# Performance work log

Measured on AMD Instinct MI355X. Metric: run time of the kernel, lower is better.

Reference implementation:

```python
import jax, jax.numpy as jnp
import numpy as np

N_NODES = 50000
N_EDGES = 800000
D_IN, D1, D2, D_OUT = 128, 150, 100, 64


def setup_inputs() -> dict:
    key = jax.random.key(0)
    ks = jax.random.split(key, 10)
    x = jax.random.normal(ks[0], (N_NODES, D_IN), dtype=jnp.float32)
    src = jax.random.randint(ks[1], (N_EDGES,), 0, N_NODES, dtype=jnp.int32)
    dst = jax.random.randint(ks[2], (N_EDGES,), 0, N_NODES, dtype=jnp.int32)
    s1 = 1.0 / np.sqrt(D_IN)
    s2 = 1.0 / np.sqrt(D1)
    s3 = 1.0 / np.sqrt(D2)
    W1 = jax.random.uniform(ks[3], (D_IN, D1), jnp.float32, -s1, s1)
    b1 = jnp.zeros((D1,), jnp.float32)
    Wn = jax.random.uniform(ks[4], (D1, D2), jnp.float32, -s2, s2)
    Ws = jax.random.uniform(ks[5], (D1, D2), jnp.float32, -s2, s2)
    b2 = jnp.zeros((D2,), jnp.float32)
    W3 = jax.random.uniform(ks[6], (D2, D_OUT), jnp.float32, -s3, s3)
    b3 = jnp.zeros((D_OUT,), jnp.float32)
    return {"x": x, "src": src, "dst": dst, "W1": W1, "b1": b1,
            "Wn": Wn, "Ws": Ws, "b2": b2, "W3": W3, "b3": b3}


def _degrees(src, dst, n):
    ones = jnp.ones(src.shape[0], jnp.float32)
    deg_out = jax.ops.segment_sum(ones, src, num_segments=n)
    deg_in = jax.ops.segment_sum(ones, dst, num_segments=n)
    return deg_out, deg_in


def reference(x, src, dst, W1, b1, Wn, Ws, b2, W3, b3):
    n = x.shape[0]
    deg_out, deg_in = _degrees(src, dst, n)
    norm_out = jax.lax.rsqrt(jnp.maximum(deg_out, 1.0))  # [N]
    norm_in = jax.lax.rsqrt(jnp.maximum(deg_in, 1.0))    # [N]

    # --- GraphConv (norm='both'): D_in^{-1/2} A D_out^{-1/2} X W + b ---
    h = x * norm_out[:, None]                                   # [N, D_IN]
    agg = jax.ops.segment_sum(h[src], dst, num_segments=n)      # [N, D_IN]
    h = (agg * norm_in[:, None]) @ W1 + b1                      # [N, D1]
    h = jax.nn.elu(h)

    # --- SAGEConv (mean): fc_self(h) + fc_neigh(mean_neighbors(h)) + b ---
    neigh_sum = jax.ops.segment_sum(h[src], dst, num_segments=n)  # [N, D1]
    neigh = neigh_sum / jnp.maximum(deg_in, 1.0)[:, None]
    h = h @ Ws + neigh @ Wn + b2                                  # [N, D2]
    h = jax.nn.elu(h)

    # --- Dense + ELU ---
    out = jax.nn.elu(h @ W3 + b3)                                 # [N, D_OUT]
    return out
```

## Files before the change

### kernel.cpp

```cpp
#include <hip/hip_runtime.h>
#include <math.h>

#define N_NODES 50000
#define N_EDGES 800000
#define D_IN 128
#define D1 150
#define LD1 152
#define D2 100
#define LDP 128
#define D_OUT 64
#define SLOT 64
#define HBLK 64
#define HBIN 12500

#define LDS_K 40

using short8 = __attribute__((ext_vector_type(8))) short;
using f32x4  = __attribute__((ext_vector_type(4))) float;

__device__ __forceinline__ float elu(float v) { return v > 0.0f ? v : expm1f(v); }

__device__ __forceinline__ void split_bf16(float a, unsigned short& h, unsigned short& l) {
    unsigned int bits = __float_as_uint(a);
    unsigned int hb = (bits + 0x8000u) >> 16;
    h = (unsigned short)hb;
    float r = a - __uint_as_float(hb << 16);
    l = (unsigned short)((__float_as_uint(r) + 0x8000u) >> 16);
}

__device__ __forceinline__ void split_store16(unsigned short* hrow, unsigned short* lrow,
                                              const float* vv) {
    short8 h0, h1v, l0, l1v;
#pragma unroll
    for (int i = 0; i < 8; ++i) {
        unsigned short hh, ll;
        split_bf16(vv[i], hh, ll);
        h0[i] = (short)hh; l0[i] = (short)ll;
    }
#pragma unroll
    for (int i = 0; i < 8; ++i) {
        unsigned short hh, ll;
        split_bf16(vv[8 + i], hh, ll);
        h1v[i] = (short)hh; l1v[i] = (short)ll;
    }
    *(short8*)(hrow) = h0;
    *(short8*)(hrow + 8) = h1v;
    *(short8*)(lrow) = l0;
    *(short8*)(lrow + 8) = l1v;
}

__global__ __launch_bounds__(256) void hist_kernel(const int* __restrict__ src,
                                                   unsigned int* __restrict__ partial) {
    __shared__ unsigned int bins[HBIN];
    int tid = threadIdx.x, b = blockIdx.x;
    for (int i = tid; i < HBIN; i += 256) bins[i] = 0u;
    __syncthreads();
    int e0 = b * (N_EDGES / HBLK);
    int e1 = e0 + (N_EDGES / HBLK);
    for (int e = e0 + tid; e < e1; e += 256) {
        int s = src[e];
        atomicAdd(&bins[s >> 2], 1u << ((s & 3) * 8));
    }
    __syncthreads();
    unsigned int* outp = partial + (size_t)b * HBIN;
    for (int i = tid; i < HBIN; i += 256) outp[i] = bins[i];
}

__global__ __launch_bounds__(256) void norm_kernel(const unsigned int* __restrict__ partial,
                                                   float* __restrict__ norm_out) {
    int i = blockIdx.x * blockDim.x + threadIdx.x;
    if (i >= HBIN) return;
    unsigned int acc = 0;
#pragma unroll
    for (int h = 0; h < HBLK; ++h) acc += partial[(size_t)h * HBIN + i];
#pragma unroll
    for (int j = 0; j < 4; ++j) {
        unsigned int dg = (acc >> (j * 8)) & 0xFF;
        norm_out[i * 4 + j] = rsqrtf(fmaxf((float)dg, 1.0f));
    }
}

__global__ void fill_kernel(const int* __restrict__ src, const int* __restrict__ dst,
                            int* __restrict__ cursor, unsigned short* __restrict__ slots) {
    int e = blockIdx.x * blockDim.x + threadIdx.x;
    if (e < N_EDGES) {
        int d = dst[e], s = src[e];
        int pos = atomicAdd(&cursor[d], 1);
        if (pos < SLOT) slots[d * SLOT + pos] = (unsigned short)s;
    }
}

__global__ __launch_bounds__(256) void gather_x(const float* __restrict__ x,
                                                const float* __restrict__ norm_out,
                                                const int* __restrict__ deg_in,
                                                const unsigned short* __restrict__ slots,
                                                float* __restrict__ agg) {
    int wave = threadIdx.x >> 6;
    int lane = threadIdx.x & 63;
    int half = lane >> 5;
    int c = lane & 31;
    int n = blockIdx.x * 4 + wave;
    if (n >= N_NODES) return;
    int beg = n * SLOT;
    int dg = deg_in[n]; if (dg > SLOT) dg = SLOT;
    int end = beg + dg;
    float4 acc = {0.0f, 0.0f, 0.0f, 0.0f};
    int e = beg + half;
    for (; e + 2 < end; e += 4) {
        int s0 = slots[e];
        int s1 = slots[e + 2];
        float w0 = norm_out[s0], w1 = norm_out[s1];
        float4 v0 = ((const float4*)(x + (size_t)s0 * D_IN))[c];
        float4 v1 = ((const float4*)(x + (size_t)s1 * D_IN))[c];
        acc.x += v0.x * w0 + v1.x * w1;
        acc.y += v0.y * w0 + v1.y * w1;
        acc.z += v0.z * w0 + v1.z * w1;
        acc.w += v0.w * w0 + v1.w * w1;
    }
    if (e < end) {
        int s = slots[e];
        float w = norm_out[s];
        float4 v = ((const float4*)(x + (size_t)s * D_IN))[c];
        acc.x += v.x * w; acc.y += v.y * w; acc.z += v.z * w; acc.w += v.w * w;
    }
    acc.x += __shfl_xor(acc.x, 32);
    acc.y += __shfl_xor(acc.y, 32);
    acc.z += __shfl_xor(acc.z, 32);
    acc.w += __shfl_xor(acc.w, 32);
    if (half == 0) ((float4*)(agg + (size_t)n * D_IN))[c] = acc;
}

__global__ __launch_bounds__(256) void gather_p(const float* __restrict__ p,
                                                const int* __restrict__ deg_in,
                                                const unsigned short* __restrict__ slots,
                                                float* __restrict__ ns) {
    int wave = threadIdx.x >> 6;
    int lane = threadIdx.x & 63;
    int half = lane >> 5;
    int c = lane & 31;
    bool cv = c < D2 / 4;
    int n = blockIdx.x * 4 + wave;
    if (n >= N_NODES) return;
    int beg = n * SLOT;
    int dg = deg_in[n]; if (dg > SLOT) dg = SLOT;
    int end = beg + dg;
    float4 acc = {0.0f, 0.0f, 0.0f, 0.0f};
    if (cv) {
        int e = beg + half;
        for (; e + 2 < end; e += 4) {
            int s0 = slots[e];
            int s1 = slots[e + 2];
            float4 v0 = ((const float4*)(p + (size_t)s0 * LDP))[c];
            float4 v1 = ((const float4*)(p + (size_t)s1 * LDP))[c];
            acc.x += v0.x + v1.x;
            acc.y += v0.y + v1.y;
            acc.z += v0.z + v1.z;
            acc.w += v0.w + v1.w;
        }
        if (e < end) {
            int s = slots[e];
            float4 v = ((const float4*)(p + (size_t)s * LDP))[c];
            acc.x += v.x; acc.y += v.y; acc.z += v.z; acc.w += v.w;
        }
    }
    acc.x += __shfl_xor(acc.x, 32);
    acc.y += __shfl_xor(acc.y, 32);
    acc.z += __shfl_xor(acc.z, 32);
    acc.w += __shfl_xor(acc.w, 32);
    if (half == 0 && cv) ((float4*)(ns + (size_t)n * LDP))[c] = acc;
}


template <int K, int KP, int NW, int LDA, int PRE, int EPI, int LDC, int GROUP>
__global__ __launch_bounds__(256, PRE ? 2 : 3)
void gemm_mfma(const float* __restrict__ A, const float* __restrict__ W,
               const float* __restrict__ nsrc, const int* __restrict__ deg,
               const float* __restrict__ bstage, const float* __restrict__ bepi,
               float* __restrict__ C) {
    constexpr int NSTEP = KP / 32;
    constexpr int MBLK = (N_NODES + 127) / 128;
    __shared__ __align__(16) unsigned short AsH[128][LDS_K];
    __shared__ __align__(16) unsigned short AsL[128][LDS_K];
    __shared__ __align__(16) unsigned short BsH[64][LDS_K];
    __shared__ __align__(16) unsigned short BsL[64][LDS_K];

    const int b = blockIdx.x;
    const int c = b & 7;
    const int sIdx = b >> 3;
    const int jj = sIdx / GROUP;
    const int yy = sIdx - jj * GROUP;
    const int xb = c + 8 * jj;
    if (xb >= MBLK) return;
    const int m0 = xb * 128;
    const int n0 = yy * 64;

    const int tid = threadIdx.x;
    const int arow = tid >> 1;
    const int af = (tid & 1) * 16;
    const int grow = m0 + arow;
    const int bn = tid & 63;
    const int bkg = tid >> 6;
    const int bcol = n0 + bn;
    const int wid = tid >> 6;
    const int lane = tid & 63;
    const int wm = (wid >> 1) * 64;
    const int wn = (wid & 1) * 32;
    const int fr = lane & 15;
    const int fg = lane >> 4;

    float invd = 1.0f;
    if (PRE) {
        int dv = (grow < N_NODES) ? deg[grow] : 1;
        invd = 1.0f / fmaxf((float)dv, 1.0f);
    }

    f32x4 acc[4][2];
#pragma unroll
    for (int i = 0; i < 4; ++i)
#pragma unroll
        for (int j = 0; j < 2; ++j) acc[i][j] = {0.0f, 0.0f, 0.0f, 0.0f};

    auto load_a = [&](int k0, float* vA, float* vN) {
        if (grow < N_NODES && k0 + 32 <= K) {
            const float* ap = A + (size_t)grow * LDA + k0 + af;
#pragma unroll
            for (int h = 0; h < 4; ++h) {
                float4 v = *(const float4*)(ap + h * 4);
                vA[h * 4 + 0] = v.x; vA[h * 4 + 1] = v.y;
                vA[h * 4 + 2] = v.z; vA[h * 4 + 3] = v.w;
            }
            if (PRE) {
                const float* np = nsrc + (size_t)grow * LDP + k0 + af;
#pragma unroll
                for (int h = 0; h < 4; ++h) {
                    float4 v = *(const float4*)(np + h * 4);
                    vN[h * 4 + 0] = v.x; vN[h * 4 + 1] = v.y;
                    vN[h * 4 + 2] = v.z; vN[h * 4 + 3] = v.w;
                }
            }
        } else {
#pragma unroll
            for (int i = 0; i < 16; ++i) {
                int k = k0 + af + i;
                bool ok = (grow < N_NODES && k < K);
                vA[i] = ok ? A[(size_t)grow * LDA + k] : 0.0f;
                if (PRE) vN[i] = ok ? nsrc[(size_t)grow * LDP + k] : 0.0f;
            }
        }
    };
    auto load_b = [&](int k0, float* vB) {
#pragma unroll
        for (int kk = 0; kk < 8; ++kk) {
            int k = k0 + bkg * 8 + kk;
            vB[kk] = (k < K && bcol < NW) ? W[(size_t)k * NW + bcol] : 0.0f;
        }
    };
    auto stage = [&](int k0, const float* vA, const float* vN, const float* vB) {
        float tv[16];
        if (!PRE) {
#pragma unroll
            for (int i = 0; i < 16; ++i) tv[i] = vA[i];
        } else if (grow < N_NODES && k0 + 32 <= K) {
#pragma unroll
            for (int i = 0; i < 16; ++i)
                tv[i] = elu(vA[i] + bstage[k0 + af + i] + vN[i] * invd);
        } else {
#pragma unroll
            for (int i = 0; i < 16; ++i) {
                int k = k0 + af + i;
                float v = 0.0f;
                if (grow < N_NODES && k < K) v = elu(vA[i] + bstage[k] + vN[i] * invd);
                tv[i] = v;
            }
        }
        split_store16(&AsH[arow][af], &AsL[arow][af], tv);
        short8 hh8, ll8;
#pragma unroll
        for (int kk = 0; kk < 8; ++kk) {
            unsigned short hh, ll;
            split_bf16(vB[kk], hh, ll);
            hh8[kk] = (short)hh; ll8[kk] = (short)ll;
        }
        *(short8*)&BsH[bn][bkg * 8] = hh8;
        *(short8*)&BsL[bn][bkg * 8] = ll8;
    };

    float bufA[2][16], bufN[2][16], bufB[2][8];
    load_a(0, bufA[0], bufN[0]);
    load_b(0, bufB[0]);

#pragma unroll
    for (int t = 0; t < NSTEP; ++t) {
        const int cur = t & 1, nxt = cur ^ 1;
        if (t + 1 < NSTEP) {
            load_a((t + 1) * 32, bufA[nxt], bufN[nxt]);
            load_b((t + 1) * 32, bufB[nxt]);
        }
        __syncthreads();
        stage(t * 32, bufA[cur], bufN[cur], bufB[cur]);
        __syncthreads();
        short8 ah[4], al[4];
#pragma unroll
        for (int fi = 0; fi < 4; ++fi) {
            ah[fi] = *(const short8*)&AsH[wm + fi * 16 + fr][fg * 8];
            al[fi] = *(const short8*)&AsL[wm + fi * 16 + fr][fg * 8];
        }
#pragma unroll
        for (int fj = 0; fj < 2; ++fj) {
            short8 bh = *(const short8*)&BsH[wn + fj * 16 + fr][fg * 8];
            short8 bl = *(const short8*)&BsL[wn + fj * 16 + fr][fg * 8];
#pragma unroll
            for (int fi = 0; fi < 4; ++fi) {
                acc[fi][fj] = __builtin_amdgcn_mfma_f32_16x16x32_bf16(ah[fi], bh, acc[fi][fj], 0, 0, 0);
                acc[fi][fj] = __builtin_amdgcn_mfma_f32_16x16x32_bf16(al[fi], bh, acc[fi][fj], 0, 0, 0);
                acc[fi][fj] = __builtin_amdgcn_mfma_f32_16x16x32_bf16(ah[fi], bl, acc[fi][fj], 0, 0, 0);
            }
        }
    }

#pragma unroll
    for (int fi = 0; fi < 4; ++fi) {
#pragma unroll
        for (int r = 0; r < 4; ++r) {
            int row = m0 + wm + fi * 16 + fg * 4 + r;
            if (row >= N_NODES) continue;
            float rmul = 1.0f;
            if (EPI == 1) rmul = rsqrtf(fmaxf((float)deg[row], 1.0f));
#pragma unroll
            for (int fj = 0; fj < 2; ++fj) {
                int col = n0 + wn + fj * 16 + fr;
                if (col >= LDC) continue;
                float v = 0.0f;
                if (col < NW) {
                    v = acc[fi][fj][r];
                    if (EPI == 1) v = elu(v * rmul + bepi[col]);
                    else if (EPI == 3) v = elu(v + bepi[col]);
                }
                C[(size_t)row * LDC + col] = v;
            }
        }
    }
}

__global__ __launch_bounds__(256, 3)
void gemm_dual_mfma(const float* __restrict__ h1, const float* __restrict__ Wn,
                    const float* __restrict__ Ws, float* __restrict__ p,
                    float* __restrict__ h2pre) {
    constexpr int NSTEP = 5;
    constexpr int MBLK = (N_NODES + 127) / 128;
    __shared__ __align__(16) unsigned short AsH[128][LDS_K];
    __shared__ __align__(16) unsigned short AsL[128][LDS_K];
    __shared__ __align__(16) unsigned short BsH[64][LDS_K];
    __shared__ __align__(16) unsigned short BsL[64][LDS_K];

    const int b = blockIdx.x;
    const int c = b & 7;
    const int sIdx = b >> 3;
    const int jj = sIdx >> 2;
    const int yy = sIdx & 3;
    const int xb = c + 8 * jj;
    if (xb >= MBLK) return;
    const int m0 = xb * 128;
    const int n0 = (yy & 1) * 64;
    const float* W = (yy < 2) ? Wn : Ws;

    const int tid = threadIdx.x;
    const int arow = tid >> 1;
    const int af = (tid & 1) * 16;
    const int grow = m0 + arow;
    const int bn = tid & 63;
    const int bkg = tid >> 6;
    const int bcol = n0 + bn;
    const int wid = tid >> 6;
    const int lane = tid & 63;
    const int wm = (wid >> 1) * 64;
    const int wn = (wid & 1) * 32;
    const int fr = lane & 15;
    const int fg = lane >> 4;

    f32x4 acc[4][2];
#pragma unroll
    for (int i = 0; i < 4; ++i)
#pragma unroll
        for (int j = 0; j < 2; ++j) acc[i][j] = {0.0f, 0.0f, 0.0f, 0.0f};

    auto load_a = [&](int k0, float* vA) {
        if (grow < N_NODES && k0 + 32 <= D1) {
            const float* ap = h1 + (size_t)grow * LD1 + k0 + af;
#pragma unroll
            for (int h = 0; h < 4; ++h) {
                float4 v = *(const float4*)(ap + h * 4);
                vA[h * 4 + 0] = v.x; vA[h * 4 + 1] = v.y;
                vA[h * 4 + 2] = v.z; vA[h * 4 + 3] = v.w;
            }
        } else {
#pragma unroll
            for (int i = 0; i < 16; ++i) {
                int k = k0 + af + i;
                vA[i] = (grow < N_NODES && k < D1) ? h1[(size_t)grow * LD1 + k] : 0.0f;
            }
        }
    };
    auto load_b = [&](int k0, float* vB) {
#pragma unroll
        for (int kk = 0; kk < 8; ++kk) {
            int k = k0 + bkg * 8 + kk;
            vB[kk] = (k < D1 && bcol < D2) ? W[(size_t)k * D2 + bcol] : 0.0f;
        }
    };
    auto stage = [&](const float* vA, const float* vB) {
        split_store16(&AsH[arow][af], &AsL[arow][af], vA);
        short8 hh8, ll8;
#pragma unroll
        for (int kk = 0; kk < 8; ++kk) {
            unsigned short hh, ll;
            split_bf16(vB[kk], hh, ll);
            hh8[kk] = (short)hh; ll8[kk] = (short)ll;
        }
        *(short8*)&BsH[bn][bkg * 8] = hh8;
        *(short8*)&BsL[bn][bkg * 8] = ll8;
    };

    float bufA[2][16], bufB[2][8];
    load_a(0, bufA[0]);
    load_b(0, bufB[0]);

#pragma unroll
    for (int t = 0; t < NSTEP; ++t) {
        const int cur = t & 1, nxt = cur ^ 1;
        if (t + 1 < NSTEP) {
            load_a((t + 1) * 32, bufA[nxt]);
            load_b((t + 1) * 32, bufB[nxt]);
        }
        __syncthreads();
        stage(bufA[cur], bufB[cur]);
        __syncthreads();
        short8 ah[4], al[4];
#pragma unroll
        for (int fi = 0; fi < 4; ++fi) {
            ah[fi] = *(const short8*)&AsH[wm + fi * 16 + fr][fg * 8];
            al[fi] = *(const short8*)&AsL[wm + fi * 16 + fr][fg * 8];
        }
#pragma unroll
        for (int fj = 0; fj < 2; ++fj) {
            short8 bh = *(const short8*)&BsH[wn + fj * 16 + fr][fg * 8];
            short8 bl = *(const short8*)&BsL[wn + fj * 16 + fr][fg * 8];
#pragma unroll
            for (int fi = 0; fi < 4; ++fi) {
                acc[fi][fj] = __builtin_amdgcn_mfma_f32_16x16x32_bf16(ah[fi], bh, acc[fi][fj], 0, 0, 0);
                acc[fi][fj] = __builtin_amdgcn_mfma_f32_16x16x32_bf16(al[fi], bh, acc[fi][fj], 0, 0, 0);
                acc[fi][fj] = __builtin_amdgcn_mfma_f32_16x16x32_bf16(ah[fi], bl, acc[fi][fj], 0, 0, 0);
            }
        }
    }

#pragma unroll
    for (int fi = 0; fi < 4; ++fi) {
#pragma unroll
        for (int r = 0; r < 4; ++r) {
            int row = m0 + wm + fi * 16 + fg * 4 + r;
            if (row >= N_NODES) continue;
#pragma unroll
            for (int fj = 0; fj < 2; ++fj) {
                int col = n0 + wn + fj * 16 + fr;
                float v = acc[fi][fj][r];
                if (yy < 2) {
                    p[(size_t)row * LDP + col] = (col < D2) ? v : 0.0f;
                } else {
                    if (col < D2) h2pre[(size_t)row * D2 + col] = v;
                }
            }
        }
    }
}

extern "C" void kernel_launch(void* const* d_in, const int* in_sizes, int n_in,
                              void* d_out, int out_size, void* d_ws, size_t ws_size,
                              hipStream_t stream) {
    const float* x  = (const float*)d_in[0];
    const int* src  = (const int*)d_in[1];
    const int* dst  = (const int*)d_in[2];
    const float* W1 = (const float*)d_in[3];
    const float* b1 = (const float*)d_in[4];
    const float* Wn = (const float*)d_in[5];
    const float* Ws = (const float*)d_in[6];
    const float* b2 = (const float*)d_in[7];
    const float* W3 = (const float*)d_in[8];
    const float* b3 = (const float*)d_in[9];
    float* out = (float*)d_out;

    char* wsb = (char*)d_ws;
    unsigned int* partial = (unsigned int*)wsb;
    int*   cursor     = (int*)wsb + 800000;
    float* norm_out   = (float*)wsb + 850000;
    unsigned short* slots = (unsigned short*)((float*)wsb + 900000);
    float* agg        = (float*)wsb + 2500000;
    float* h1         = (float*)wsb + 8900000;
    float* h2pre      = (float*)wsb + 16500000;
    float* p          = agg;
    float* ns         = h1;
    int*   deg_in     = cursor;

    hipMemsetAsync(cursor, 0, N_NODES * sizeof(int), stream);

    hist_kernel<<<HBLK, 256, 0, stream>>>(src, partial);
    fill_kernel<<<(N_EDGES + 255) / 256, 256, 0, stream>>>(src, dst, cursor, slots);
    norm_kernel<<<(HBIN + 255) / 256, 256, 0, stream>>>(partial, norm_out);
    gather_x<<<(N_NODES + 3) / 4, 256, 0, stream>>>(x, norm_out, deg_in, slots, agg);

    const int MB = (N_NODES + 127) / 128;
    const int XG = (MB + 7) / 8;
    gemm_mfma<128, 128, 150, 128, 0, 1, LD1, 3><<<XG * 8 * 3, 256, 0, stream>>>(
        agg, W1, nullptr, deg_in, nullptr, b1, h1);
    gemm_dual_mfma<<<XG * 8 * 4, 256, 0, stream>>>(h1, Wn, Ws, p, h2pre);
    gather_p<<<(N_NODES + 3) / 4, 256, 0, stream>>>(p, deg_in, slots, ns);
    gemm_mfma<100, 128, 64, 100, 1, 3, D_OUT, 1><<<XG * 8, 256, 0, stream>>>(
        h2pre, W3, ns, deg_in, b2, b3, out);
}
```

Before: 375.9 us.

## Shrink GEMM M-tile to 64 rows and raise occupancy to four blocks

Both MFMA GEMM kernels switch from 128-row to 64-row tiles. Each wave now computes a 2x2 grid of 16x16 fragments, and the launch bound rises to 4 blocks per CU. Per-thread A loads are reshaped to 8 contiguous floats, and __syncthreads is replaced by an inline-asm lgkmcnt wait plus s_barrier with a scheduling barrier. The aim is more blocks and more waves in flight on these memory-bound, skinny GEMMs. The cost is halved B-tile reuse per block, so W is loaded and split twice as often per output row.

```diff
diff --git a/kernel.cpp b/kernel.cpp
--- a/kernel.cpp
+++ b/kernel.cpp
@@ -28,25 +28,30 @@
     l = (unsigned short)((__float_as_uint(r) + 0x8000u) >> 16);
 }
 
-__device__ __forceinline__ void split_store16(unsigned short* hrow, unsigned short* lrow,
-                                              const float* vv) {
-    short8 h0, h1v, l0, l1v;
+__device__ __forceinline__ void split8(const float4 a, const float4 b, short8& h, short8& l) {
+    float f[8] = {a.x, a.y, a.z, a.w, b.x, b.y, b.z, b.w};
 #pragma unroll
     for (int i = 0; i < 8; ++i) {
         unsigned short hh, ll;
-        split_bf16(vv[i], hh, ll);
-        h0[i] = (short)hh; l0[i] = (short)ll;
-    }
-#pragma unroll
-    for (int i = 0; i < 8; ++i) {
-        unsigned short hh, ll;
-        split_bf16(vv[8 + i], hh, ll);
-        h1v[i] = (short)hh; l1v[i] = (short)ll;
-    }
-    *(short8*)(hrow) = h0;
-    *(short8*)(hrow + 8) = h1v;
-    *(short8*)(lrow) = l0;
-    *(short8*)(lrow + 8) = l1v;
+        split_bf16(f[i], hh, ll);
+        h[i] = (short)hh; l[i] = (short)ll;
+    }
+}
+
+__device__ __forceinline__ float4 g_load4(const float* p) { return *(const float4*)p; }
+
+__device__ __forceinline__ float4 g_load4_guard(const float* row, int kbase, int Klim, bool rowok) {
+    float4 v;
+    v.x = (rowok && kbase + 0 < Klim) ? row[kbase + 0] : 0.0f;
+    v.y = (rowok && kbase + 1 < Klim) ? row[kbase + 1] : 0.0f;
+    v.z = (rowok && kbase + 2 < Klim) ? row[kbase + 2] : 0.0f;
+    v.w = (rowok && kbase + 3 < Klim) ? row[kbase + 3] : 0.0f;
+    return v;
+}
+
+__device__ __forceinline__ void barrier_lgkm() {
+    asm volatile("s_waitcnt lgkmcnt(0)\n\ts_barrier" ::: "memory");
+    __builtin_amdgcn_sched_barrier(0);
 }
 
 __global__ __launch_bounds__(256) void hist_kernel(const int* __restrict__ src,
@@ -172,154 +177,176 @@
 
 
 template <int K, int KP, int NW, int LDA, int PRE, int EPI, int LDC, int GROUP>
-__global__ __launch_bounds__(256, PRE ? 2 : 3)
+__global__ __launch_bounds__(256, 4)
 void gemm_mfma(const float* __restrict__ A, const float* __restrict__ W,
                const float* __restrict__ nsrc, const int* __restrict__ deg,
                const float* __restrict__ bstage, const float* __restrict__ bepi,
                float* __restrict__ C) {
     constexpr int NSTEP = KP / 32;
-    constexpr int MBLK = (N_NODES + 127) / 128;
-    __shared__ __align__(16) unsigned short AsH[128][LDS_K];
-    __shared__ __align__(16) unsigned short AsL[128][LDS_K];
+    constexpr int MBLK = (N_NODES + 63) / 64;
+    __shared__ __align__(16) unsigned short AsH[64][LDS_K];
+    __shared__ __align__(16) unsigned short AsL[64][LDS_K];
     __shared__ __align__(16) unsigned short BsH[64][LDS_K];
     __shared__ __align__(16) unsigned short BsL[64][LDS_K];
 
     const int b = blockIdx.x;
-    const int c = b & 7;
+    const int cxcd = b & 7;
     const int sIdx = b >> 3;
     const int jj = sIdx / GROUP;
     const int yy = sIdx - jj * GROUP;
-    const int xb = c + 8 * jj;
+    const int xb = cxcd + 8 * jj;
     if (xb >= MBLK) return;
-    const int m0 = xb * 128;
+    const int m0 = xb * 64;
     const int n0 = yy * 64;
 
     const int tid = threadIdx.x;
-    const int arow = tid >> 1;
-    const int af = (tid & 1) * 16;
+    const int arow = tid >> 2;
+    const int ak = (tid & 3) * 8;
     const int grow = m0 + arow;
+    const bool rowok = grow < N_NODES;
     const int bn = tid & 63;
     const int bkg = tid >> 6;
     const int bcol = n0 + bn;
     const int wid = tid >> 6;
     const int lane = tid & 63;
-    const int wm = (wid >> 1) * 64;
+    const int wm = (wid >> 1) * 32;
     const int wn = (wid & 1) * 32;
     const int fr = lane & 15;
     const int fg = lane >> 4;
 
     float invd = 1.0f;
     if (PRE) {
-        int dv = (grow < N_NODES) ? deg[grow] : 1;
+        int dv = rowok ? deg[grow] : 1;
         invd = 1.0f / fmaxf((float)dv, 1.0f);
     }
 
-    f32x4 acc[4][2];
-#pragma unroll
-    for (int i = 0; i < 4; ++i)
+    f32x4 acc[2][2];
+#pragma unroll
+    for (int i = 0; i < 2; ++i)
 #pragma unroll
         for (int j = 0; j < 2; ++j) acc[i][j] = {0.0f, 0.0f, 0.0f, 0.0f};
 
-    auto load_a = [&](int k0, float* vA, float* vN) {
-        if (grow < N_NODES && k0 + 32 <= K) {
-            const float* ap = A + (size_t)grow * LDA + k0 + af;
-#pragma unroll
-            for (int h = 0; h < 4; ++h) {
-                float4 v = *(const float4*)(ap + h * 4);
-                vA[h * 4 + 0] = v.x; vA[h * 4 + 1] = v.y;
-                vA[h * 4 + 2] = v.z; vA[h * 4 + 3] = v.w;
-            }
-            if (PRE) {
-                const float* np = nsrc + (size_t)grow * LDP + k0 + af;
-#pragma unroll
-                for (int h = 0; h < 4; ++h) {
-                    float4 v = *(const float4*)(np + h * 4);
-                    vN[h * 4 + 0] = v.x; vN[h * 4 + 1] = v.y;
-                    vN[h * 4 + 2] = v.z; vN[h * 4 + 3] = v.w;
-                }
-            }
+    const float* arp = A + (size_t)grow * LDA;
+    const float* nrp = PRE ? (nsrc + (size_t)grow * LDP) : nullptr;
+
+    float4 pa[2][2], pn[2][2];
+    float pb[2][8];
+
+    {
+        if (rowok && 32 <= K) {
+            pa[0][0] = g_load4(arp + ak);
+            pa[0][1] = g_load4(arp + ak + 4);
         } else {
-#pragma unroll
-            for (int i = 0; i < 16; ++i) {
-                int k = k0 + af + i;
-                bool ok = (grow < N_NODES && k < K);
-                vA[i] = ok ? A[(size_t)grow * LDA + k] : 0.0f;
-                if (PRE) vN[i] = ok ? nsrc[(size_t)grow * LDP + k] : 0.0f;
-            }
-        }
-    };
-    auto load_b = [&](int k0, float* vB) {
+            pa[0][0] = g_load4_guard(arp, ak, K, rowok);
+            pa[0][1] = g_load4_guard(arp, ak + 4, K, rowok);
+        }
+        if (PRE) {
+            if (rowok && 32 <= K) {
+                pn[0][0] = g_load4(nrp + ak);
+                pn[0][1] = g_load4(nrp + ak + 4);
+            } else {
+                pn[0][0] = g_load4_guard(nrp, ak, K, rowok);
+                pn[0][1] = g_load4_guard(nrp, ak + 4, K, rowok);
+            }
+        }
 #pragma unroll
         for (int kk = 0; kk < 8; ++kk) {
-            int k = k0 + bkg * 8 + kk;
-            vB[kk] = (k < K && bcol < NW) ? W[(size_t)k * NW + bcol] : 0.0f;
-        }
-    };
-    auto stage = [&](int k0, const float* vA, const float* vN, const float* vB) {
-        float tv[16];
-        if (!PRE) {
-#pragma unroll
-            for (int i = 0; i < 16; ++i) tv[i] = vA[i];
-        } else if (grow < N_NODES && k0 + 32 <= K) {
-#pragma unroll
-            for (int i = 0; i < 16; ++i)
-                tv[i] = elu(vA[i] + bstage[k0 + af + i] + vN[i] * invd);
-        } else {
-#pragma unroll
-            for (int i = 0; i < 16; ++i) {
-                int k = k0 + af + i;
-                float v = 0.0f;
-                if (grow < N_NODES && k < K) v = elu(vA[i] + bstage[k] + vN[i] * invd);
-                tv[i] = v;
-            }
-        }
-        split_store16(&AsH[arow][af], &AsL[arow][af], tv);
-        short8 hh8, ll8;
-#pragma unroll
-        for (int kk = 0; kk < 8; ++kk) {
-            unsigned short hh, ll;
-            split_bf16(vB[kk], hh, ll);
-            hh8[kk] = (short)hh; ll8[kk] = (short)ll;
-        }
-        *(short8*)&BsH[bn][bkg * 8] = hh8;
-        *(short8*)&BsL[bn][bkg * 8] = ll8;
-    };
-
-    float bufA[2][16], bufN[2][16], bufB[2][8];
-    load_a(0, bufA[0], bufN[0]);
-    load_b(0, bufB[0]);
+            int k = bkg * 8 + kk;
+            pb[0][kk] = (k < K && bcol < NW) ? W[(size_t)k * NW + bcol] : 0.0f;
+        }
+    }
 
 #pragma unroll
     for (int t = 0; t < NSTEP; ++t) {
         const int cur = t & 1, nxt = cur ^ 1;
         if (t + 1 < NSTEP) {
-            load_a((t + 1) * 32, bufA[nxt], bufN[nxt]);
-            load_b((t + 1) * 32, bufB[nxt]);
-        }
-        __syncthreads();
-        stage(t * 32, bufA[cur], bufN[cur], bufB[cur]);
-        __syncthreads();
-        short8 ah[4], al[4];
-#pragma unroll
-        for (int fi = 0; fi < 4; ++fi) {
-            ah[fi] = *(const short8*)&AsH[wm + fi * 16 + fr][fg * 8];
-            al[fi] = *(const short8*)&AsL[wm + fi * 16 + fr][fg * 8];
-        }
-#pragma unroll
-        for (int fj = 0; fj < 2; ++fj) {
-            short8 bh = *(const short8*)&BsH[wn + fj * 16 + fr][fg * 8];
-            short8 bl = *(const short8*)&BsL[wn + fj * 16 + fr][fg * 8];
-#pragma unroll
-            for (int fi = 0; fi < 4; ++fi) {
-                acc[fi][fj] = __builtin_amdgcn_mfma_f32_16x16x32_bf16(ah[fi], bh, acc[fi][fj], 0, 0, 0);
-                acc[fi][fj] = __builtin_amdgcn_mfma_f32_16x16x32_bf16(al[fi], bh, acc[fi][fj], 0, 0, 0);
-                acc[fi][fj] = __builtin_amdgcn_mfma_f32_16x16x32_bf16(ah[fi], bl, acc[fi][fj], 0, 0, 0);
-            }
-        }
-    }
-
-#pragma unroll
-    for (int fi = 0; fi < 4; ++fi) {
+            const int k0n = (t + 1) * 32;
+            if (rowok && k0n + 32 <= K) {
+                pa[nxt][0] = g_load4(arp + k0n + ak);
+                pa[nxt][1] = g_load4(arp + k0n + ak + 4);
+            } else {
+                pa[nxt][0] = g_load4_guard(arp, k0n + ak, K, rowok);
+                pa[nxt][1] = g_load4_guard(arp, k0n + ak + 4, K, rowok);
+            }
+            if (PRE) {
+                if (rowok && k0n + 32 <= K) {
+                    pn[nxt][0] = g_load4(nrp + k0n + ak);
+                    pn[nxt][1] = g_load4(nrp + k0n + ak + 4);
+                } else {
+                    pn[nxt][0] = g_load4_guard(nrp, k0n + ak, K, rowok);
+                    pn[nxt][1] = g_load4_guard(nrp, k0n + ak + 4, K, rowok);
+                }
+            }
+#pragma unroll
+            for (int kk = 0; kk < 8; ++kk) {
+                int k = k0n + bkg * 8 + kk;
+                pb[nxt][kk] = (k < K && bcol < NW) ? W[(size_t)k * NW + bcol] : 0.0f;
+            }
+        }
+        barrier_lgkm();
+        {
+            const int k0 = t * 32;
+            float4 va0 = pa[cur][0], va1 = pa[cur][1];
+            if (PRE) {
+                const float4 vn0 = pn[cur][0], vn1 = pn[cur][1];
+                if (k0 + 32 <= K) {
+                    va0.x = elu(va0.x + bstage[k0 + ak + 0] + vn0.x * invd);
+                    va0.y = elu(va0.y + bstage[k0 + ak + 1] + vn0.y * invd);
+                    va0.z = elu(va0.z + bstage[k0 + ak + 2] + vn0.z * invd);
+                    va0.w = elu(va0.w + bstage[k0 + ak + 3] + vn0.w * invd);
+                    va1.x = elu(va1.x + bstage[k0 + ak + 4] + vn1.x * invd);
+                    va1.y = elu(va1.y + bstage[k0 + ak + 5] + vn1.y * invd);
+                    va1.z = elu(va1.z + bstage[k0 + ak + 6] + vn1.z * invd);
+                    va1.w = elu(va1.w + bstage[k0 + ak + 7] + vn1.w * invd);
+                } else {
+                    va0.x = (k0 + ak + 0 < K) ? elu(va0.x + bstage[k0 + ak + 0] + vn0.x * invd) : 0.0f;
+                    va0.y = (k0 + ak + 1 < K) ? elu(va0.y + bstage[k0 + ak + 1] + vn0.y * invd) : 0.0f;
+                    va0.z = (k0 + ak + 2 < K) ? elu(va0.z + bstage[k0 + ak + 2] + vn0.z * invd) : 0.0f;
+                    va0.w = (k0 + ak + 3 < K) ? elu(va0.w + bstage[k0 + ak + 3] + vn0.w * invd) : 0.0f;
+                    va1.x = (k0 + ak + 4 < K) ? elu(va1.x + bstage[k0 + ak + 4] + vn1.x * invd) : 0.0f;
+                    va1.y = (k0 + ak + 5 < K) ? elu(va1.y + bstage[k0 + ak + 5] + vn1.y * invd) : 0.0f;
+                    va1.z = (k0 + ak + 6 < K) ? elu(va1.z + bstage[k0 + ak + 6] + vn1.z * invd) : 0.0f;
+                    va1.w = (k0 + ak + 7 < K) ? elu(va1.w + bstage[k0 + ak + 7] + vn1.w * invd) : 0.0f;
+                }
+            }
+            short8 h8, l8;
+            split8(va0, va1, h8, l8);
+            *(short8*)&AsH[arow][ak] = h8;
+            *(short8*)&AsL[arow][ak] = l8;
+            float4 vb0, vb1;
+            vb0.x = pb[cur][0]; vb0.y = pb[cur][1]; vb0.z = pb[cur][2]; vb0.w = pb[cur][3];
+            vb1.x = pb[cur][4]; vb1.y = pb[cur][5]; vb1.z = pb[cur][6]; vb1.w = pb[cur][7];
+            split8(vb0, vb1, h8, l8);
+            *(short8*)&BsH[bn][bkg * 8] = h8;
+            *(short8*)&BsL[bn][bkg * 8] = l8;
+        }
+        barrier_lgkm();
+        {
+            short8 ah0 = *(const short8*)&AsH[wm + fr][fg * 8];
+            short8 ah1 = *(const short8*)&AsH[wm + 16 + fr][fg * 8];
+            short8 al0 = *(const short8*)&AsL[wm + fr][fg * 8];
+            short8 al1 = *(const short8*)&AsL[wm + 16 + fr][fg * 8];
+            short8 bh0 = *(const short8*)&BsH[wn + fr][fg * 8];
+            short8 bh1 = *(const short8*)&BsH[wn + 16 + fr][fg * 8];
+            short8 bl0 = *(const short8*)&BsL[wn + fr][fg * 8];
+            short8 bl1 = *(const short8*)&BsL[wn + 16 + fr][fg * 8];
+            acc[0][0] = __builtin_amdgcn_mfma_f32_16x16x32_bf16(ah0, bh0, acc[0][0], 0, 0, 0);
+            acc[0][0] = __builtin_amdgcn_mfma_f32_16x16x32_bf16(al0, bh0, acc[0][0], 0, 0, 0);
+            acc[0][0] = __builtin_amdgcn_mfma_f32_16x16x32_bf16(ah0, bl0, acc[0][0], 0, 0, 0);
+            acc[0][1] = __builtin_amdgcn_mfma_f32_16x16x32_bf16(ah0, bh1, acc[0][1], 0, 0, 0);
+            acc[0][1] = __builtin_amdgcn_mfma_f32_16x16x32_bf16(al0, bh1, acc[0][1], 0, 0, 0);
+            acc[0][1] = __builtin_amdgcn_mfma_f32_16x16x32_bf16(ah0, bl1, acc[0][1], 0, 0, 0);
+            acc[1][0] = __builtin_amdgcn_mfma_f32_16x16x32_bf16(ah1, bh0, acc[1][0], 0, 0, 0);
+            acc[1][0] = __builtin_amdgcn_mfma_f32_16x16x32_bf16(al1, bh0, acc[1][0], 0, 0, 0);
+            acc[1][0] = __builtin_amdgcn_mfma_f32_16x16x32_bf16(ah1, bl0, acc[1][0], 0, 0, 0);
+            acc[1][1] = __builtin_amdgcn_mfma_f32_16x16x32_bf16(ah1, bh1, acc[1][1], 0, 0, 0);
+            acc[1][1] = __builtin_amdgcn_mfma_f32_16x16x32_bf16(al1, bh1, acc[1][1], 0, 0, 0);
+            acc[1][1] = __builtin_amdgcn_mfma_f32_16x16x32_bf16(ah1, bl1, acc[1][1], 0, 0, 0);
+        }
+    }
+
+#pragma unroll
+    for (int fi = 0; fi < 2; ++fi) {
 #pragma unroll
         for (int r = 0; r < 4; ++r) {
             int row = m0 + wm + fi * 16 + fg * 4 + r;
@@ -342,120 +369,127 @@
     }
 }
 
-__global__ __launch_bounds__(256, 3)
+__global__ __launch_bounds__(256, 4)
 void gemm_dual_mfma(const float* __restrict__ h1, const float* __restrict__ Wn,
                     const float* __restrict__ Ws, float* __restrict__ p,
                     float* __restrict__ h2pre) {
     constexpr int NSTEP = 5;
-    constexpr int MBLK = (N_NODES + 127) / 128;
-    __shared__ __align__(16) unsigned short AsH[128][LDS_K];
-    __shared__ __align__(16) unsigned short AsL[128][LDS_K];
+    constexpr int MBLK = (N_NODES + 63) / 64;
+    __shared__ __align__(16) unsigned short AsH[64][LDS_K];
+    __shared__ __align__(16) unsigned short AsL[64][LDS_K];
     __shared__ __align__(16) unsigned short BsH[64][LDS_K];
     __shared__ __align__(16) unsigned short BsL[64][LDS_K];
 
     const int b = blockIdx.x;
-    const int c = b & 7;
+    const int cxcd = b & 7;
     const int sIdx = b >> 3;
     const int jj = sIdx >> 2;
     const int yy = sIdx & 3;
-    const int xb = c + 8 * jj;
+    const int xb = cxcd + 8 * jj;
     if (xb >= MBLK) return;
-    const int m0 = xb * 128;
+    const int m0 = xb * 64;
     const int n0 = (yy & 1) * 64;
     const float* W = (yy < 2) ? Wn : Ws;
 
     const int tid = threadIdx.x;
-    const int arow = tid >> 1;
-    const int af = (tid & 1) * 16;
+    const int arow = tid >> 2;
+    const int ak = (tid & 3) * 8;
     const int grow = m0 + arow;
+    const bool rowok = grow < N_NODES;
     const int bn = tid & 63;
     const int bkg = tid >> 6;
     const int bcol = n0 + bn;
     const int wid = tid >> 6;
     const int lane = tid & 63;
-    const int wm = (wid >> 1) * 64;
+    const int wm = (wid >> 1) * 32;
     const int wn = (wid & 1) * 32;
     const int fr = lane & 15;
     const int fg = lane >> 4;
 
-    f32x4 acc[4][2];
-#pragma unroll
-    for (int i = 0; i < 4; ++i)
+    f32x4 acc[2][2];
+#pragma unroll
+    for (int i = 0; i < 2; ++i)
 #pragma unroll
         for (int j = 0; j < 2; ++j) acc[i][j] = {0.0f, 0.0f, 0.0f, 0.0f};
 
-    auto load_a = [&](int k0, float* vA) {
-        if (grow < N_NODES && k0 + 32 <= D1) {
-            const float* ap = h1 + (size_t)grow * LD1 + k0 + af;
-#pragma unroll
-            for (int h = 0; h < 4; ++h) {
-                float4 v = *(const float4*)(ap + h * 4);
-                vA[h * 4 + 0] = v.x; vA[h * 4 + 1] = v.y;
-                vA[h * 4 + 2] = v.z; vA[h * 4 + 3] = v.w;
-            }
+    const float* arp = h1 + (size_t)grow * LD1;
+
+    float4 pa[2][2];
+    float pb[2][8];
+
+    {
+        if (rowok) {
+            pa[0][0] = g_load4(arp + ak);
+            pa[0][1] = g_load4(arp + ak + 4);
         } else {
-#pragma unroll
-            for (int i = 0; i < 16; ++i) {
-                int k = k0 + af + i;
-                vA[i] = (grow < N_NODES && k < D1) ? h1[(size_t)grow * LD1 + k] : 0.0f;
-            }
-        }
-    };
-    auto load_b = [&](int k0, float* vB) {
+            pa[0][0] = g_load4_guard(arp, ak, D1, rowok);
+            pa[0][1] = g_load4_guard(arp, ak + 4, D1, rowok);
+        }
 #pragma unroll
         for (int kk = 0; kk < 8; ++kk) {
-            int k = k0 + bkg * 8 + kk;
-            vB[kk] = (k < D1 && bcol < D2) ? W[(size_t)k * D2 + bcol] : 0.0f;
-        }
-    };
-    auto stage = [&](const float* vA, const float* vB) {
-        split_store16(&AsH[arow][af], &AsL[arow][af], vA);
-        short8 hh8, ll8;
-#pragma unroll
-        for (int kk = 0; kk < 8; ++kk) {
-            unsigned short hh, ll;
-            split_bf16(vB[kk], hh, ll);
-            hh8[kk] = (short)hh; ll8[kk] = (short)ll;
-        }
-        *(short8*)&BsH[bn][bkg * 8] = hh8;
-        *(short8*)&BsL[bn][bkg * 8] = ll8;
-    };
-
-    float bufA[2][16], bufB[2][8];
-    load_a(0, bufA[0]);
-    load_b(0, bufB[0]);
+            int k = bkg * 8 + kk;
+            pb[0][kk] = (k < D1 && bcol < D2) ? W[(size_t)k * D2 + bcol] : 0.0f;
+        }
+    }
 
 #pragma unroll
     for (int t = 0; t < NSTEP; ++t) {
         const int cur = t & 1, nxt = cur ^ 1;
         if (t + 1 < NSTEP) {
-            load_a((t + 1) * 32, bufA[nxt]);
-            load_b((t + 1) * 32, bufB[nxt]);
-        }
-        __syncthreads();
-        stage(bufA[cur], bufB[cur]);
-        __syncthreads();
-        short8 ah[4], al[4];
-#pragma unroll
-        for (int fi = 0; fi < 4; ++fi) {
-            ah[fi] = *(const short8*)&AsH[wm + fi * 16 + fr][fg * 8];
-            al[fi] = *(const short8*)&AsL[wm + fi * 16 + fr][fg * 8];
-        }
-#pragma unroll
-        for (int fj = 0; fj < 2; ++fj) {
-            short8 bh = *(const short8*)&BsH[wn + fj * 16 + fr][fg * 8];
-            short8 bl = *(const short8*)&BsL[wn + fj * 16 + fr][fg * 8];
-#pragma unroll
-            for (int fi = 0; fi < 4; ++fi) {
-                acc[fi][fj] = __builtin_amdgcn_mfma_f32_16x16x32_bf16(ah[fi], bh, acc[fi][fj], 0, 0, 0);
-                acc[fi][fj] = __builtin_amdgcn_mfma_f32_16x16x32_bf16(al[fi], bh, acc[fi][fj], 0, 0, 0);
-                acc[fi][fj] = __builtin_amdgcn_mfma_f32_16x16x32_bf16(ah[fi], bl, acc[fi][fj], 0, 0, 0);
-            }
-        }
-    }
-
-#pragma unroll
-    for (int fi = 0; fi < 4; ++fi) {
+            const int k0n = (t + 1) * 32;
+            if (rowok && k0n + 32 <= D1) {
+                pa[nxt][0] = g_load4(arp + k0n + ak);
+                pa[nxt][1] = g_load4(arp + k0n + ak + 4);
+            } else {
+                pa[nxt][0] = g_load4_guard(arp, k0n + ak, D1, rowok);
+                pa[nxt][1] = g_load4_guard(arp, k0n + ak + 4, D1, rowok);
+            }
+#pragma unroll
+            for (int kk = 0; kk < 8; ++kk) {
+                int k = k0n + bkg * 8 + kk;
+                pb[nxt][kk] = (k < D1 && bcol < D2) ? W[(size_t)k * D2 + bcol] : 0.0f;
+            }
+        }
+        barrier_lgkm();
+        {
+            short8 h8, l8;
+            split8(pa[cur][0], pa[cur][1], h8, l8);
+            *(short8*)&AsH[arow][ak] = h8;
+            *(short8*)&AsL[arow][ak] = l8;
+            float4 vb0, vb1;
+            vb0.x = pb[cur][0]; vb0.y = pb[cur][1]; vb0.z = pb[cur][2]; vb0.w = pb[cur][3];
+            vb1.x = pb[cur][4]; vb1.y = pb[cur][5]; vb1.z = pb[cur][6]; vb1.w = pb[cur][7];
+            split8(vb0, vb1, h8, l8);
+            *(short8*)&BsH[bn][bkg * 8] = h8;
+            *(short8*)&BsL[bn][bkg * 8] = l8;
+        }
+        barrier_lgkm();
+        {
+            short8 ah0 = *(const short8*)&AsH[wm + fr][fg * 8];
+            short8 ah1 = *(const short8*)&AsH[wm + 16 + fr][fg * 8];
+            short8 al0 = *(const short8*)&AsL[wm + fr][fg * 8];
+            short8 al1 = *(const short8*)&AsL[wm + 16 + fr][fg * 8];
+            short8 bh0 = *(const short8*)&BsH[wn + fr][fg * 8];
+            short8 bh1 = *(const short8*)&BsH[wn + 16 + fr][fg * 8];
+            short8 bl0 = *(const short8*)&BsL[wn + fr][fg * 8];
+            short8 bl1 = *(const short8*)&BsL[wn + 16 + fr][fg * 8];
+            acc[0][0] = __builtin_amdgcn_mfma_f32_16x16x32_bf16(ah0, bh0, acc[0][0], 0, 0, 0);
+            acc[0][0] = __builtin_amdgcn_mfma_f32_16x16x32_bf16(al0, bh0, acc[0][0], 0, 0, 0);
+            acc[0][0] = __builtin_amdgcn_mfma_f32_16x16x32_bf16(ah0, bl0, acc[0][0], 0, 0, 0);
+            acc[0][1] = __builtin_amdgcn_mfma_f32_16x16x32_bf16(ah0, bh1, acc[0][1], 0, 0, 0);
+            acc[0][1] = __builtin_amdgcn_mfma_f32_16x16x32_bf16(al0, bh1, acc[0][1], 0, 0, 0);
+            acc[0][1] = __builtin_amdgcn_mfma_f32_16x16x32_bf16(ah0, bl1, acc[0][1], 0, 0, 0);
+            acc[1][0] = __builtin_amdgcn_mfma_f32_16x16x32_bf16(ah1, bh0, acc[1][0], 0, 0, 0);
+            acc[1][0] = __builtin_amdgcn_mfma_f32_16x16x32_bf16(al1, bh0, acc[1][0], 0, 0, 0);
+            acc[1][0] = __builtin_amdgcn_mfma_f32_16x16x32_bf16(ah1, bl0, acc[1][0], 0, 0, 0);
+            acc[1][1] = __builtin_amdgcn_mfma_f32_16x16x32_bf16(ah1, bh1, acc[1][1], 0, 0, 0);
+            acc[1][1] = __builtin_amdgcn_mfma_f32_16x16x32_bf16(al1, bh1, acc[1][1], 0, 0, 0);
+            acc[1][1] = __builtin_amdgcn_mfma_f32_16x16x32_bf16(ah1, bl1, acc[1][1], 0, 0, 0);
+        }
+    }
+
+#pragma unroll
+    for (int fi = 0; fi < 2; ++fi) {
 #pragma unroll
         for (int r = 0; r < 4; ++r) {
             int row = m0 + wm + fi * 16 + fg * 4 + r;
@@ -508,7 +542,7 @@
     norm_kernel<<<(HBIN + 255) / 256, 256, 0, stream>>>(partial, norm_out);
     gather_x<<<(N_NODES + 3) / 4, 256, 0, stream>>>(x, norm_out, deg_in, slots, agg);
 
-    const int MB = (N_NODES + 127) / 128;
+    const int MB = (N_NODES + 63) / 64;
     const int XG = (MB + 7) / 8;
     gemm_mfma<128, 128, 150, 128, 0, 1, LD1, 3><<<XG * 8 * 3, 256, 0, stream>>>(
         agg, W1, nullptr, deg_in, nullptr, b1, h1);
```

Measured after the change: 341.1 us. -9.3%, faster.
